# Kernel tuning notes

Measured on AMD Instinct MI355X. Metric: run time of the kernel, lower is better.

The kernel has to match this reference:

```python
import jax, jax.numpy as jnp
import numpy as np

D_MODEL = 512
NUM_HEADS = 8
D_K = D_MODEL // NUM_HEADS
D_FF = 4 * D_MODEL
EPS = 1e-5


def _pos_encoding(seq_len, d_model, dtype=jnp.float32):
    pos = jnp.arange(seq_len, dtype=jnp.float32)[:, None]              # [S,1]
    div = jnp.exp(jnp.arange(0, d_model, 2, dtype=jnp.float32) * (-np.log(10000.0) / d_model))  # [D/2]
    ang = pos * div                                                      # [S,D/2]
    pe = jnp.stack([jnp.sin(ang), jnp.cos(ang)], axis=-1).reshape(seq_len, d_model)
    return pe.astype(dtype)


def _layernorm(x, g, b):
    mu = jnp.mean(x, axis=-1, keepdims=True)
    var = jnp.mean(jnp.square(x - mu), axis=-1, keepdims=True)
    return (x - mu) * jax.lax.rsqrt(var + EPS) * g + b


def setup_inputs() -> dict:
    key = jax.random.key(0)
    ks = jax.random.split(key, 12)
    B, S, D = 4, 2048, D_MODEL
    s = 1.0 / np.sqrt(D)
    inp = {
        "x": jax.random.normal(ks[0], (B, S, D), jnp.float32),
        "Wq": jax.random.normal(ks[1], (D, D), jnp.float32) * s,
        "bq": jnp.zeros((D,), jnp.float32),
        "Wk": jax.random.normal(ks[2], (D, D), jnp.float32) * s,
        "bk": jnp.zeros((D,), jnp.float32),
        "Wv": jax.random.normal(ks[3], (D, D), jnp.float32) * s,
        "bv": jnp.zeros((D,), jnp.float32),
        "Wo": jax.random.normal(ks[4], (D, D), jnp.float32) * s,
        "bo": jnp.zeros((D,), jnp.float32),
        "g1": jnp.ones((D,), jnp.float32),
        "b1": jnp.zeros((D,), jnp.float32),
        "W_ff1": jax.random.normal(ks[5], (D, D_FF), jnp.float32) * s,
        "b_ff1": jnp.zeros((D_FF,), jnp.float32),
        "W_ff2": jax.random.normal(ks[6], (D_FF, D), jnp.float32) * (1.0 / np.sqrt(D_FF)),
        "b_ff2": jnp.zeros((D,), jnp.float32),
        "g2": jnp.ones((D,), jnp.float32),
        "b2": jnp.zeros((D,), jnp.float32),
    }
    return inp


def reference(x, Wq, bq, Wk, bk, Wv, bv, Wo, bo, g1, b1, W_ff1, b_ff1, W_ff2, b_ff2, g2, b2):
    B, S, D = x.shape
    H, dk = NUM_HEADS, D_K
    # positional encoding (deterministic buffer)
    x = x + _pos_encoding(S, D, x.dtype)[None]
    # projections -> [B,H,S,dk]
    q = (x @ Wq + bq).reshape(B, S, H, dk).transpose(0, 2, 1, 3)
    k = (x @ Wk + bk).reshape(B, S, H, dk).transpose(0, 2, 1, 3)
    v = (x @ Wv + bv).reshape(B, S, H, dk).transpose(0, 2, 1, 3)
    # naive attention: materialized [B,H,S,S] scores (as in original)
    scores = jnp.einsum('bhqd,bhkd->bhqk', q, k) / np.sqrt(dk)
    attn = jax.nn.softmax(scores, axis=-1)
    ctx = jnp.einsum('bhqk,bhkd->bhqd', attn, v)
    ctx = ctx.transpose(0, 2, 1, 3).reshape(B, S, D)
    attn_out = ctx @ Wo + bo
    # residual + LN + FFN + residual + LN
    h = _layernorm(x + attn_out, g1, b1)
    ff = jax.nn.relu(h @ W_ff1 + b_ff1) @ W_ff2 + b_ff2
    return _layernorm(h + ff, g2, b2)
```

## Files before the change

kernel.cpp:

```cpp
#include <hip/hip_runtime.h>

typedef unsigned short u16;
typedef unsigned int u32;
typedef __attribute__((ext_vector_type(8))) short s16x8;
typedef __attribute__((ext_vector_type(2))) float f32x2;
typedef __attribute__((ext_vector_type(4))) float f32x4;
typedef __attribute__((ext_vector_type(16))) float f32x16;
typedef __attribute__((ext_vector_type(2))) u32 u32x2;
typedef __attribute__((ext_vector_type(4))) u32 u32x4;

#define MB (1ull << 20)
#define K1SCALE 0.18033688f

__device__ __forceinline__ u16 f2bf(float f) {
  u32 u = __float_as_uint(f);
  u32 r = (u + 0x7fffu + ((u >> 16) & 1u)) >> 16;
  return (u16)r;
}

__device__ __forceinline__ float bf2f(u16 x) { return __uint_as_float(((u32)x) << 16); }

__device__ __forceinline__ u32 cvtpk(float lo, float hi) {
  u32 r;
  asm("v_cvt_pk_bf16_f32 %0, %1, %2" : "=v"(r) : "v"(lo), "v"(hi));
  return r;
}

__device__ __forceinline__ f32x2 pk_add(f32x2 a, f32x2 b) {
  f32x2 d;
  asm("v_pk_add_f32 %0, %1, %2" : "=v"(d) : "v"(a), "v"(b));
  return d;
}

__device__ __forceinline__ void gload16(const u16* g, u16* l) {
  __builtin_amdgcn_global_load_lds((const __attribute__((address_space(1))) void*)g,
                                   (__attribute__((address_space(3))) void*)l, 16, 0, 0);
}

__global__ __launch_bounds__(256) void k_posenc(const float* __restrict__ x,
                                                float* __restrict__ xf, u16* __restrict__ xb) {
  int idx = blockIdx.x * 256 + threadIdx.x;
  int i2 = idx & 255;
  int srow = (idx >> 8) & 2047;
  float div = __expf((float)i2 * -0.03597789207803196f);
  float ang = (float)srow * div;
  f32x2 xv = *(const f32x2*)&x[(size_t)idx * 2];
  float v0 = xv[0] + __sinf(ang);
  float v1 = xv[1] + __cosf(ang);
  *(f32x2*)&xf[(size_t)idx * 2] = (f32x2){v0, v1};
  *(u32*)&xb[(size_t)idx * 2] = cvtpk(v0, v1);
}

__global__ __launch_bounds__(256) void k_wprep(const float* __restrict__ Wq, const float* __restrict__ Wk,
                                               const float* __restrict__ Wv, const float* __restrict__ Wo,
                                               const float* __restrict__ Wff1, const float* __restrict__ Wff2,
                                               const float* __restrict__ bq, const float* __restrict__ bk,
                                               const float* __restrict__ bv,
                                               u16* __restrict__ WqkvT, u16* __restrict__ WoT,
                                               u16* __restrict__ Wff1T, u16* __restrict__ Wff2T,
                                               float* __restrict__ bqkv) {
  __shared__ float tile[32][33];
  int id = blockIdx.x;
  if (id >= 3072) {
    int j = (id - 3072) * 256 + threadIdx.x;
    float v = (j < 512) ? bq[j] * K1SCALE : ((j < 1024) ? bk[j - 512] : bv[j - 1024]);
    bqkv[j] = v;
    return;
  }
  const float* W;
  u16* Wt;
  int K, N, k0, n0;
  float sc = 1.0f;
  if (id < 1024) {
    int mi = id >> 8, t = id & 255;
    K = 512; N = 512;
    k0 = (t & 15) * 32;
    n0 = (t >> 4) * 32;
    if (mi == 0) { W = Wq; Wt = WqkvT; sc = K1SCALE; }
    else if (mi == 1) { W = Wk; Wt = WqkvT + 512 * 512; }
    else if (mi == 2) { W = Wv; Wt = WqkvT + 2 * 512 * 512; }
    else { W = Wo; Wt = WoT; }
  } else if (id < 2048) {
    int t = id - 1024;
    K = 512; N = 2048;
    k0 = (t & 15) * 32;
    n0 = (t >> 4) * 32;
    W = Wff1; Wt = Wff1T;
  } else {
    int t = id - 2048;
    K = 2048; N = 512;
    k0 = (t >> 4) * 32;
    n0 = (t & 15) * 32;
    W = Wff2; Wt = Wff2T;
  }
  int tx = threadIdx.x & 31, ty = threadIdx.x >> 5;
  #pragma unroll
  for (int i = 0; i < 32; i += 8)
    tile[ty + i][tx] = W[(size_t)(k0 + ty + i) * N + n0 + tx];
  __syncthreads();
  #pragma unroll
  for (int i = 0; i < 32; i += 8)
    Wt[(size_t)(n0 + ty + i) * K + k0 + tx] = f2bf(tile[tx][ty + i] * sc);
}

template <int NK, bool RELU, bool QKV, bool F32OUT>
__global__ __launch_bounds__(512, 2) void k_gemm3(const u16* __restrict__ A, const u16* __restrict__ Bt,
                                                  const float* __restrict__ bias, u16* __restrict__ Cb,
                                                  u16* __restrict__ vTout,
                                                  float* __restrict__ Cf0, float* __restrict__ Cf1,
                                                  int N, int lda) {
  constexpr int K = NK * 64;
  __shared__ u16 lA[3][256 * 64];
  __shared__ u16 lB[3][128 * 64];
  int t = threadIdx.x;
  int lane = t & 63;
  int w = t >> 6;
  int wr = w >> 1, wc = w & 1;
  int g = lane >> 4, c = lane & 15;
  size_t tm = (size_t)blockIdx.x * 256;
  size_t tn = (size_t)blockIdx.y * 128;
  A += (size_t)blockIdx.z * K;
  Bt += (size_t)blockIdx.z * K;

  auto stg = [&](int buf, int kt, int half) {
    int k0 = kt * 64;
    #pragma unroll
    for (int i = 0; i < 2; i++) {
      int ch = t + (half * 2 + i) * 512;
      int row = ch >> 3;
      int koff = ((ch ^ row) & 7) << 3;
      gload16(A + (tm + row) * lda + k0 + koff, &lA[buf][ch * 8]);
    }
    int ch = t + half * 512;
    int row = ch >> 3;
    int koff = ((ch ^ row) & 7) << 3;
    gload16(Bt + (tn + row) * lda + k0 + koff, &lB[buf][ch * 8]);
  };

  f32x4 acc[4][4];
  #pragma unroll
  for (int i = 0; i < 4; i++)
    #pragma unroll
    for (int j = 0; j < 4; j++) acc[i][j] = (f32x4){0.f, 0.f, 0.f, 0.f};

  stg(0, 0, 0); stg(0, 0, 1);
  stg(1, 1, 0); stg(1, 1, 1);
  asm volatile("s_waitcnt vmcnt(6)" ::: "memory");
  __builtin_amdgcn_s_barrier();
  __builtin_amdgcn_sched_barrier(0);

  #pragma unroll
  for (int kt = 0; kt < NK; kt++) {
    const int buf = kt % 3;
    const int nb = (kt + 2) % 3;
    s16x8 bfr[4][2], afr[2][2];
    #pragma unroll
    for (int nr = 0; nr < 4; nr++)
      #pragma unroll
      for (int ks = 0; ks < 2; ks++)
        bfr[nr][ks] = *(const s16x8*)&lB[buf][(wc * 64 + nr * 16 + c) * 64 + (((g + 4 * ks) ^ (c & 7)) << 3)];
    #pragma unroll
    for (int mr = 0; mr < 2; mr++)
      #pragma unroll
      for (int ks = 0; ks < 2; ks++)
        afr[mr][ks] = *(const s16x8*)&lA[buf][(wr * 64 + mr * 16 + c) * 64 + (((g + 4 * ks) ^ (c & 7)) << 3)];
    if (kt + 2 < NK) stg(nb, kt + 2, 0);
    __builtin_amdgcn_s_barrier();
    __builtin_amdgcn_sched_barrier(0);
    __builtin_amdgcn_s_setprio(1);
    #pragma unroll
    for (int mr = 0; mr < 2; mr++)
      #pragma unroll
      for (int nr = 0; nr < 4; nr++)
        #pragma unroll
        for (int ks = 0; ks < 2; ks++)
          acc[mr][nr] = __builtin_amdgcn_mfma_f32_16x16x32_bf16(afr[mr][ks], bfr[nr][ks], acc[mr][nr], 0, 0, 0);
    __builtin_amdgcn_s_setprio(0);
    __builtin_amdgcn_s_barrier();
    __builtin_amdgcn_sched_barrier(0);
    #pragma unroll
    for (int mr = 0; mr < 2; mr++)
      #pragma unroll
      for (int ks = 0; ks < 2; ks++)
        afr[mr][ks] = *(const s16x8*)&lA[buf][(wr * 64 + (mr + 2) * 16 + c) * 64 + (((g + 4 * ks) ^ (c & 7)) << 3)];
    if (kt + 2 < NK) stg(nb, kt + 2, 1);
    __builtin_amdgcn_s_barrier();
    __builtin_amdgcn_sched_barrier(0);
    __builtin_amdgcn_s_setprio(1);
    #pragma unroll
    for (int mr = 0; mr < 2; mr++)
      #pragma unroll
      for (int nr = 0; nr < 4; nr++)
        #pragma unroll
        for (int ks = 0; ks < 2; ks++)
          acc[mr + 2][nr] = __builtin_amdgcn_mfma_f32_16x16x32_bf16(afr[mr][ks], bfr[nr][ks], acc[mr + 2][nr], 0, 0, 0);
    __builtin_amdgcn_s_setprio(0);
    if (kt < NK - 1) {
      if (kt + 2 < NK)
        asm volatile("s_waitcnt vmcnt(6)" ::: "memory");
      else
        asm volatile("s_waitcnt vmcnt(0)" ::: "memory");
      __builtin_amdgcn_s_barrier();
      __builtin_amdgcn_sched_barrier(0);
    }
  }

  if (QKV && tn >= 1024) {
    #pragma unroll
    for (int mr = 0; mr < 4; mr++) {
      int row0 = (int)tm + wr * 64 + mr * 16 + g * 4;
      int b = row0 >> 11, s0 = row0 & 2047;
      #pragma unroll
      for (int nr = 0; nr < 4; nr++) {
        int colr = (int)(tn - 1024) + wc * 64 + nr * 16 + c;
        int h = colr >> 6, d = colr & 63;
        float bv = bias[1024 + colr];
        u32 w0 = cvtpk(acc[mr][nr][0] + bv, acc[mr][nr][1] + bv);
        u32 w1 = cvtpk(acc[mr][nr][2] + bv, acc[mr][nr][3] + bv);
        u32x2 pp = {w0, w1};
        *(u32x2*)&vTout[((size_t)((b << 3) + h) * 64 + d) * 2048 + s0] = pp;
      }
    }
  } else if (F32OUT) {
    float* Cf = blockIdx.z ? Cf1 : Cf0;
    bool addb = (blockIdx.z == 0);
    #pragma unroll
    for (int nr = 0; nr < 4; nr++) {
      size_t col = tn + wc * 64 + nr * 16 + c;
      float bv = addb ? bias[col] : 0.0f;
      #pragma unroll
      for (int mr = 0; mr < 4; mr++) {
        size_t row0 = tm + wr * 64 + mr * 16 + g * 4;
        #pragma unroll
        for (int r = 0; r < 4; r++) Cf[(row0 + r) * N + col] = acc[mr][nr][r] + bv;
      }
    }
  } else {
    #pragma unroll
    for (int nr = 0; nr < 4; nr++) {
      size_t col = tn + wc * 64 + nr * 16 + c;
      float bv = bias[col];
      #pragma unroll
      for (int mr = 0; mr < 4; mr++) {
        size_t row0 = tm + wr * 64 + mr * 16 + g * 4;
        #pragma unroll
        for (int r = 0; r < 4; r++) {
          float v = acc[mr][nr][r] + bv;
          if (RELU) v = fmaxf(v, 0.0f);
          Cb[(row0 + r) * N + col] = f2bf(v);
        }
      }
    }
  }
}

template <int BN, bool RELU, bool WF32, bool WBF16>
__global__ __launch_bounds__(256) void k_gemm(const u16* __restrict__ A, const u16* __restrict__ Bt,
                                              const float* __restrict__ bias,
                                              float* __restrict__ Cf, u16* __restrict__ Cb,
                                              int N, int K) {
  constexpr int NACC = BN / 32;
  __shared__ u16 lA[128 * 64];
  __shared__ u16 lB[BN * 64];
  int t = threadIdx.x;
  int lane = t & 63;
  int w = t >> 6;
  int wm = w >> 1, wn = w & 1;
  int g = lane >> 4, c = lane & 15;
  size_t tm = (size_t)blockIdx.x * 128;
  size_t tn = (size_t)blockIdx.y * BN;

  f32x4 acc[4][NACC];
  #pragma unroll
  for (int i = 0; i < 4; i++)
    #pragma unroll
    for (int j = 0; j < NACC; j++) acc[i][j] = (f32x4){0.f, 0.f, 0.f, 0.f};

  for (int k0 = 0; k0 < K; k0 += 64) {
    __syncthreads();
    #pragma unroll
    for (int i = 0; i < 4; i++) {
      int ch = t + i * 256;
      int row = ch >> 3;
      int koff = ((ch ^ row) & 7) << 3;
      gload16(A + (tm + row) * K + k0 + koff, lA + ch * 8);
    }
    #pragma unroll
    for (int i = 0; i < BN / 32; i++) {
      int ch = t + i * 256;
      int row = ch >> 3;
      int koff = ((ch ^ row) & 7) << 3;
      gload16(Bt + (tn + row) * K + k0 + koff, lB + ch * 8);
    }
    __syncthreads();
    #pragma unroll
    for (int kh = 0; kh < 2; kh++) {
      int sl = ((g + 4 * kh) ^ (c & 7)) << 3;
      s16x8 af[4], bf[NACC];
      #pragma unroll
      for (int i = 0; i < 4; i++)
        af[i] = *(const s16x8*)&lA[(wm * 64 + i * 16 + c) * 64 + sl];
      #pragma unroll
      for (int j = 0; j < NACC; j++)
        bf[j] = *(const s16x8*)&lB[(wn * (BN / 2) + j * 16 + c) * 64 + sl];
      #pragma unroll
      for (int i = 0; i < 4; i++)
        #pragma unroll
        for (int j = 0; j < NACC; j++)
          acc[i][j] = __builtin_amdgcn_mfma_f32_16x16x32_bf16(af[i], bf[j], acc[i][j], 0, 0, 0);
    }
  }
  #pragma unroll
  for (int j = 0; j < NACC; j++) {
    size_t col = tn + wn * (BN / 2) + j * 16 + c;
    float bv = bias[col];
    #pragma unroll
    for (int i = 0; i < 4; i++) {
      size_t row0 = tm + wm * 64 + i * 16 + g * 4;
      #pragma unroll
      for (int r = 0; r < 4; r++) {
        float v = acc[i][j][r] + bv;
        if (RELU) v = fmaxf(v, 0.0f);
        if (WF32) Cf[(row0 + r) * N + col] = v;
        if (WBF16) Cb[(row0 + r) * N + col] = f2bf(v);
      }
    }
  }
}

union F16U {
  f32x16 v;
  f32x2 p[8];
};

__global__ __launch_bounds__(512, 4) void k_attn(const u16* __restrict__ qkv,
                                                 const u16* __restrict__ vT,
                                                 u16* __restrict__ ctx) {
  __shared__ u16 lds[8][4096];
  int t = threadIdx.x;
  int w = t >> 6, lane = t & 63;
  int qg = w >> 1, kh = w & 1;
  int ql = lane & 31, hi = lane >> 5;
  int bh = blockIdx.y;
  int b = bh >> 3, h = bh & 7;
  int q0 = blockIdx.x * 128 + qg * 32;
  int r7 = ql & 7;

  int sh = t >> 8;
  int th = t & 255;
  const u16* kbaseg = qkv + (size_t)(b * 2048 + sh * 1024) * 1536 + 512 + h * 64;
  const u16* vbaseg = vT + (size_t)(bh * 64) * 2048 + sh * 1024;

  auto stage = [&](int buf, int step) {
    int t0 = step * 64;
    #pragma unroll
    for (int i = 0; i < 2; i++) {
      int ch = th + i * 256;
      int row = ch >> 3;
      int off = ((ch ^ row) & 7) << 3;
      gload16(kbaseg + (size_t)(t0 + row) * 1536 + off, &lds[(sh * 2 + buf) * 2][ch * 8]);
      gload16(vbaseg + (size_t)row * 2048 + t0 + off, &lds[(sh * 2 + buf) * 2 + 1][ch * 8]);
    }
  };

  const u16* qbase = qkv + (size_t)(b * 2048 + q0 + ql) * 1536 + h * 64 + hi * 8;
  s16x8 qf[4];
  #pragma unroll
  for (int ks = 0; ks < 4; ks++) qf[ks] = *(const s16x8*)(qbase + ks * 16);

  float l = 0.f;
  F16U O0, O1;
  #pragma unroll
  for (int i = 0; i < 16; i++) { O0.v[i] = 0.f; O1.v[i] = 0.f; }

  stage(0, 0);

  for (int step = 0; step < 16; ++step) {
    int buf = step & 1;
    asm volatile("s_waitcnt vmcnt(0)" ::: "memory");
    __builtin_amdgcn_s_barrier();
    __builtin_amdgcn_sched_barrier(0);
    if (step < 15) stage(buf ^ 1, step + 1);

    const u16* lK = lds[(kh * 2 + buf) * 2];
    const u16* lV = lds[(kh * 2 + buf) * 2 + 1];

    F16U S0, S1;
    #pragma unroll
    for (int i = 0; i < 16; i++) { S0.v[i] = 0.f; S1.v[i] = 0.f; }
    #pragma unroll
    for (int ks = 0; ks < 4; ks++) {
      int so = ((ks * 2 + hi) ^ r7) << 3;
      s16x8 kf0 = *(const s16x8*)&lK[ql * 64 + so];
      s16x8 kf1 = *(const s16x8*)&lK[(32 + ql) * 64 + so];
      S0.v = __builtin_amdgcn_mfma_f32_32x32x16_bf16(kf0, qf[ks], S0.v, 0, 0, 0);
      S1.v = __builtin_amdgcn_mfma_f32_32x32x16_bf16(kf1, qf[ks], S1.v, 0, 0, 0);
    }

    #pragma unroll
    for (int i = 0; i < 16; i++) {
      S0.v[i] = __builtin_amdgcn_exp2f(S0.v[i]);
      S1.v[i] = __builtin_amdgcn_exp2f(S1.v[i]);
    }
    f32x2 c0 = pk_add(S0.p[0], S0.p[1]);
    f32x2 c1 = pk_add(S0.p[2], S0.p[3]);
    f32x2 c2 = pk_add(S0.p[4], S0.p[5]);
    f32x2 c3 = pk_add(S0.p[6], S0.p[7]);
    f32x2 d0 = pk_add(S1.p[0], S1.p[1]);
    f32x2 d1 = pk_add(S1.p[2], S1.p[3]);
    f32x2 d2 = pk_add(S1.p[4], S1.p[5]);
    f32x2 d3 = pk_add(S1.p[6], S1.p[7]);
    c0 = pk_add(c0, c1);
    c2 = pk_add(c2, c3);
    d0 = pk_add(d0, d1);
    d2 = pk_add(d2, d3);
    c0 = pk_add(c0, c2);
    d0 = pk_add(d0, d2);
    c0 = pk_add(c0, d0);
    float pssum = c0[0] + c0[1];
    pssum += __shfl_xor(pssum, 32, 64);
    l += pssum;

    auto pv = [&](const f32x16& sv, int kb) {
      u32 a0w = cvtpk(sv[0], sv[1]), a1w = cvtpk(sv[2], sv[3]);
      u32 a2w = cvtpk(sv[4], sv[5]), a3w = cvtpk(sv[6], sv[7]);
      u32 b0w = cvtpk(sv[8], sv[9]), b1w = cvtpk(sv[10], sv[11]);
      u32 b2w = cvtpk(sv[12], sv[13]), b3w = cvtpk(sv[14], sv[15]);
      asm("v_permlane32_swap_b32 %0, %1" : "+v"(a0w), "+v"(a2w));
      asm("v_permlane32_swap_b32 %0, %1" : "+v"(a1w), "+v"(a3w));
      asm("v_permlane32_swap_b32 %0, %1" : "+v"(b0w), "+v"(b2w));
      asm("v_permlane32_swap_b32 %0, %1" : "+v"(b1w), "+v"(b3w));
      u32x4 w0v = {a0w, a1w, a2w, a3w};
      u32x4 w1v = {b0w, b1w, b2w, b3w};
      s16x8 pf0 = __builtin_bit_cast(s16x8, w0v);
      s16x8 pf1 = __builtin_bit_cast(s16x8, w1v);
      int base0 = ((kb * 4 + hi) ^ r7) << 3;
      int base1 = ((kb * 4 + 2 + hi) ^ r7) << 3;
      s16x8 vf00 = *(const s16x8*)&lV[ql * 64 + base0];
      s16x8 vf01 = *(const s16x8*)&lV[ql * 64 + base1];
      s16x8 vf10 = *(const s16x8*)&lV[(32 + ql) * 64 + base0];
      s16x8 vf11 = *(const s16x8*)&lV[(32 + ql) * 64 + base1];
      O0.v = __builtin_amdgcn_mfma_f32_32x32x16_bf16(vf00, pf0, O0.v, 0, 0, 0);
      O0.v = __builtin_amdgcn_mfma_f32_32x32x16_bf16(vf01, pf1, O0.v, 0, 0, 0);
      O1.v = __builtin_amdgcn_mfma_f32_32x32x16_bf16(vf10, pf0, O1.v, 0, 0, 0);
      O1.v = __builtin_amdgcn_mfma_f32_32x32x16_bf16(vf11, pf1, O1.v, 0, 0, 0);
    };
    pv(S0.v, 0);
    pv(S1.v, 1);
  }

  asm volatile("s_waitcnt lgkmcnt(0)" ::: "memory");
  __builtin_amdgcn_s_barrier();
  float* mrg = (float*)&lds[0][0];
  float* p = mrg + (size_t)(qg * 64 + lane) * 34;
  if (kh == 1) {
    p[0] = l;
    #pragma unroll
    for (int i = 0; i < 16; i++) {
      p[1 + i] = O0.v[i];
      p[17 + i] = O1.v[i];
    }
  }
  asm volatile("s_waitcnt lgkmcnt(0)" ::: "memory");
  __builtin_amdgcn_s_barrier();
  if (kh == 0) {
    float inv = 1.0f / (l + p[0]);
    size_t obase = (size_t)(b * 2048 + q0 + ql) * 512 + h * 64;
    #pragma unroll
    for (int k = 0; k < 4; k++) {
      float v0 = (O0.v[4 * k] + p[1 + 4 * k]) * inv;
      float v1 = (O0.v[4 * k + 1] + p[1 + 4 * k + 1]) * inv;
      float v2 = (O0.v[4 * k + 2] + p[1 + 4 * k + 2]) * inv;
      float v3 = (O0.v[4 * k + 3] + p[1 + 4 * k + 3]) * inv;
      u32x2 p0 = {cvtpk(v0, v1), cvtpk(v2, v3)};
      *(u32x2*)&ctx[obase + 8 * k + 4 * hi] = p0;
      float u0 = (O1.v[4 * k] + p[17 + 4 * k]) * inv;
      float u1 = (O1.v[4 * k + 1] + p[17 + 4 * k + 1]) * inv;
      float u2 = (O1.v[4 * k + 2] + p[17 + 4 * k + 2]) * inv;
      float u3 = (O1.v[4 * k + 3] + p[17 + 4 * k + 3]) * inv;
      u32x2 p1 = {cvtpk(u0, u1), cvtpk(u2, u3)};
      *(u32x2*)&ctx[obase + 32 + 8 * k + 4 * hi] = p1;
    }
  }
}

template <bool WB>
__global__ __launch_bounds__(256) void k_addln(const float* __restrict__ A, const float* __restrict__ Bv,
                                               const float* __restrict__ G, const float* __restrict__ Bb,
                                               float* __restrict__ Of, u16* __restrict__ Ob) {
  int row = blockIdx.x;
  int t = threadIdx.x;
  size_t base = (size_t)row * 512 + 2 * t;
  f32x2 av = *(const f32x2*)&A[base];
  f32x2 bv = *(const f32x2*)&Bv[base];
  float x0 = av[0] + bv[0];
  float x1 = av[1] + bv[1];
  float s = x0 + x1;
  #pragma unroll
  for (int d = 1; d < 64; d <<= 1) s += __shfl_xor(s, d, 64);
  __shared__ float red[8];
  int w = t >> 6, lane = t & 63;
  if (lane == 0) red[w] = s;
  __syncthreads();
  float mu = (red[0] + red[1] + red[2] + red[3]) * (1.0f / 512.0f);
  float d0 = x0 - mu, d1 = x1 - mu;
  float vs = d0 * d0 + d1 * d1;
  #pragma unroll
  for (int d = 1; d < 64; d <<= 1) vs += __shfl_xor(vs, d, 64);
  if (lane == 0) red[4 + w] = vs;
  __syncthreads();
  float var = (red[4] + red[5] + red[6] + red[7]) * (1.0f / 512.0f);
  float rs = rsqrtf(var + 1e-5f);
  f32x2 gg = *(const f32x2*)&G[2 * t];
  f32x2 bb = *(const f32x2*)&Bb[2 * t];
  float o0 = d0 * rs * gg[0] + bb[0];
  float o1 = d1 * rs * gg[1] + bb[1];
  *(f32x2*)&Of[base] = (f32x2){o0, o1};
  if (WB) *(u32*)&Ob[base] = cvtpk(o0, o1);
}

__global__ __launch_bounds__(256) void k_addln3(const float* __restrict__ A, const float* __restrict__ B1,
                                                const float* __restrict__ B2,
                                                const float* __restrict__ G, const float* __restrict__ Bb,
                                                float* __restrict__ Of) {
  int row = blockIdx.x;
  int t = threadIdx.x;
  size_t base = (size_t)row * 512 + 2 * t;
  f32x2 av = *(const f32x2*)&A[base];
  f32x2 b1v = *(const f32x2*)&B1[base];
  f32x2 b2v = *(const f32x2*)&B2[base];
  float x0 = av[0] + b1v[0] + b2v[0];
  float x1 = av[1] + b1v[1] + b2v[1];
  float s = x0 + x1;
  #pragma unroll
  for (int d = 1; d < 64; d <<= 1) s += __shfl_xor(s, d, 64);
  __shared__ float red[8];
  int w = t >> 6, lane = t & 63;
  if (lane == 0) red[w] = s;
  __syncthreads();
  float mu = (red[0] + red[1] + red[2] + red[3]) * (1.0f / 512.0f);
  float d0 = x0 - mu, d1 = x1 - mu;
  float vs = d0 * d0 + d1 * d1;
  #pragma unroll
  for (int d = 1; d < 64; d <<= 1) vs += __shfl_xor(vs, d, 64);
  if (lane == 0) red[4 + w] = vs;
  __syncthreads();
  float var = (red[4] + red[5] + red[6] + red[7]) * (1.0f / 512.0f);
  float rs = rsqrtf(var + 1e-5f);
  f32x2 gg = *(const f32x2*)&G[2 * t];
  f32x2 bb = *(const f32x2*)&Bb[2 * t];
  float o0 = d0 * rs * gg[0] + bb[0];
  float o1 = d1 * rs * gg[1] + bb[1];
  *(f32x2*)&Of[base] = (f32x2){o0, o1};
}

extern "C" void kernel_launch(void* const* d_in, const int* in_sizes, int n_in,
                              void* d_out, int out_size, void* d_ws, size_t ws_size,
                              hipStream_t stream) {
  const float* x = (const float*)d_in[0];
  const float* Wq = (const float*)d_in[1];
  const float* bq = (const float*)d_in[2];
  const float* Wk = (const float*)d_in[3];
  const float* bk = (const float*)d_in[4];
  const float* Wv = (const float*)d_in[5];
  const float* bv = (const float*)d_in[6];
  const float* Wo = (const float*)d_in[7];
  const float* bo = (const float*)d_in[8];
  const float* g1 = (const float*)d_in[9];
  const float* b1 = (const float*)d_in[10];
  const float* Wff1 = (const float*)d_in[11];
  const float* bff1 = (const float*)d_in[12];
  const float* Wff2 = (const float*)d_in[13];
  const float* bff2 = (const float*)d_in[14];
  const float* g2 = (const float*)d_in[15];
  const float* b2 = (const float*)d_in[16];

  char* ws = (char*)d_ws;
  float* xpe_f = (float*)(ws + 0);
  float* ao2 = (float*)(ws + 0);
  u16* xpe_b = (u16*)(ws + 16 * MB);
  u16* qkv = (u16*)(ws + 24 * MB);
  u16* vT = (u16*)(ws + 48 * MB);
  u16* ctx = (u16*)(ws + 56 * MB);
  float* ao = (float*)(ws + 64 * MB);
  float* hf = (float*)(ws + 80 * MB);
  u16* hb = (u16*)(ws + 96 * MB);
  u16* ff1 = (u16*)(ws + 24 * MB);
  u16* WqkvT = (u16*)(ws + 104 * MB);
  u16* WoT = (u16*)(ws + 106 * MB);
  u16* Wff1T = (u16*)(ws + 107 * MB);
  u16* Wff2T = (u16*)(ws + 109 * MB);
  float* bqkv = (float*)(ws + 111 * MB);
  (void)in_sizes; (void)n_in; (void)out_size; (void)ws_size;

  k_posenc<<<8192, 256, 0, stream>>>(x, xpe_f, xpe_b);
  k_wprep<<<3078, 256, 0, stream>>>(Wq, Wk, Wv, Wo, Wff1, Wff2, bq, bk, bv,
                                    WqkvT, WoT, Wff1T, Wff2T, bqkv);

  k_gemm3<8, false, true, false><<<dim3(32, 12), 512, 0, stream>>>(xpe_b, WqkvT, bqkv, qkv, vT,
                                                                   nullptr, nullptr, 1536, 512);
  k_attn<<<dim3(16, 32), 512, 0, stream>>>(qkv, vT, ctx);
  k_gemm<64, false, true, false><<<dim3(64, 8), 256, 0, stream>>>(ctx, WoT, bo, ao, nullptr, 512, 512);
  k_addln<true><<<8192, 256, 0, stream>>>(xpe_f, ao, g1, b1, hf, hb);
  k_gemm3<8, true, false, false><<<dim3(32, 16), 512, 0, stream>>>(hb, Wff1T, bff1, ff1, nullptr,
                                                                   nullptr, nullptr, 2048, 512);
  k_gemm3<16, false, false, true><<<dim3(32, 4, 2), 512, 0, stream>>>(ff1, Wff2T, bff2, nullptr, nullptr,
                                                                      ao, ao2, 512, 2048);
  k_addln3<<<8192, 256, 0, stream>>>(hf, ao, ao2, g2, b2, (float*)d_out);
}
```

Baseline: 175.9 us.

## Merge prep kernels and remap workgroup IDs for XCD-aware L2 locality

Merges the positional-encoding and weight-prep kernels into a single launch, removing one kernel launch. Remaps the flat workgroup index in the GEMM and attention kernels so that consecutive logical tiles land on the same XCD, since blocks are dispatched round-robin across the eight XCDs on MI300-class parts. Blocks that share A/B rows or K/V heads should then hit the same L2. The remap assumes the grid size is divisible by 8, and the attention remap hardcodes 512 blocks.

```diff
diff --git a/kernel.cpp b/kernel.cpp
--- a/kernel.cpp
+++ b/kernel.cpp
@@ -18,8 +18,6 @@
   return (u16)r;
 }
 
-__device__ __forceinline__ float bf2f(u16 x) { return __uint_as_float(((u32)x) << 16); }
-
 __device__ __forceinline__ u32 cvtpk(float lo, float hi) {
   u32 r;
   asm("v_cvt_pk_bf16_f32 %0, %1, %2" : "=v"(r) : "v"(lo), "v"(hi));
@@ -37,30 +35,32 @@
                                    (__attribute__((address_space(3))) void*)l, 16, 0, 0);
 }
 
-__global__ __launch_bounds__(256) void k_posenc(const float* __restrict__ x,
-                                                float* __restrict__ xf, u16* __restrict__ xb) {
-  int idx = blockIdx.x * 256 + threadIdx.x;
-  int i2 = idx & 255;
-  int srow = (idx >> 8) & 2047;
-  float div = __expf((float)i2 * -0.03597789207803196f);
-  float ang = (float)srow * div;
-  f32x2 xv = *(const f32x2*)&x[(size_t)idx * 2];
-  float v0 = xv[0] + __sinf(ang);
-  float v1 = xv[1] + __cosf(ang);
-  *(f32x2*)&xf[(size_t)idx * 2] = (f32x2){v0, v1};
-  *(u32*)&xb[(size_t)idx * 2] = cvtpk(v0, v1);
-}
-
-__global__ __launch_bounds__(256) void k_wprep(const float* __restrict__ Wq, const float* __restrict__ Wk,
-                                               const float* __restrict__ Wv, const float* __restrict__ Wo,
-                                               const float* __restrict__ Wff1, const float* __restrict__ Wff2,
-                                               const float* __restrict__ bq, const float* __restrict__ bk,
-                                               const float* __restrict__ bv,
-                                               u16* __restrict__ WqkvT, u16* __restrict__ WoT,
-                                               u16* __restrict__ Wff1T, u16* __restrict__ Wff2T,
-                                               float* __restrict__ bqkv) {
+__global__ __launch_bounds__(256) void k_prep(const float* __restrict__ x,
+                                              float* __restrict__ xf, u16* __restrict__ xb,
+                                              const float* __restrict__ Wq, const float* __restrict__ Wk,
+                                              const float* __restrict__ Wv, const float* __restrict__ Wo,
+                                              const float* __restrict__ Wff1, const float* __restrict__ Wff2,
+                                              const float* __restrict__ bq, const float* __restrict__ bk,
+                                              const float* __restrict__ bv,
+                                              u16* __restrict__ WqkvT, u16* __restrict__ WoT,
+                                              u16* __restrict__ Wff1T, u16* __restrict__ Wff2T,
+                                              float* __restrict__ bqkv) {
   __shared__ float tile[32][33];
-  int id = blockIdx.x;
+  int bid = blockIdx.x;
+  if (bid < 8192) {
+    int idx = bid * 256 + threadIdx.x;
+    int i2 = idx & 255;
+    int srow = (idx >> 8) & 2047;
+    float div = __expf((float)i2 * -0.03597789207803196f);
+    float ang = (float)srow * div;
+    f32x2 xv = *(const f32x2*)&x[(size_t)idx * 2];
+    float v0 = xv[0] + __sinf(ang);
+    float v1 = xv[1] + __cosf(ang);
+    *(f32x2*)&xf[(size_t)idx * 2] = (f32x2){v0, v1};
+    *(u32*)&xb[(size_t)idx * 2] = cvtpk(v0, v1);
+    return;
+  }
+  int id = bid - 8192;
   if (id >= 3072) {
     int j = (id - 3072) * 256 + threadIdx.x;
     float v = (j < 512) ? bq[j] * K1SCALE : ((j < 1024) ? bk[j - 512] : bv[j - 1024]);
@@ -117,8 +117,13 @@
   int w = t >> 6;
   int wr = w >> 1, wc = w & 1;
   int g = lane >> 4, c = lane & 15;
-  size_t tm = (size_t)blockIdx.x * 256;
-  size_t tn = (size_t)blockIdx.y * 128;
+  int nwg = gridDim.x * gridDim.y;
+  int fid = blockIdx.y * gridDim.x + blockIdx.x;
+  int wid = (fid & 7) * (nwg >> 3) + (fid >> 3);
+  int bx = wid / gridDim.y;
+  int by = wid % gridDim.y;
+  size_t tm = (size_t)bx * 256;
+  size_t tn = (size_t)by * 128;
   A += (size_t)blockIdx.z * K;
   Bt += (size_t)blockIdx.z * K;
 
@@ -267,8 +272,13 @@
   int w = t >> 6;
   int wm = w >> 1, wn = w & 1;
   int g = lane >> 4, c = lane & 15;
-  size_t tm = (size_t)blockIdx.x * 128;
-  size_t tn = (size_t)blockIdx.y * BN;
+  int nwg = gridDim.x * gridDim.y;
+  int fid = blockIdx.y * gridDim.x + blockIdx.x;
+  int wid = (fid & 7) * (nwg >> 3) + (fid >> 3);
+  int bx = wid / gridDim.y;
+  int by = wid % gridDim.y;
+  size_t tm = (size_t)bx * 128;
+  size_t tn = (size_t)by * BN;
 
   f32x4 acc[4][NACC];
   #pragma unroll
@@ -341,9 +351,12 @@
   int w = t >> 6, lane = t & 63;
   int qg = w >> 1, kh = w & 1;
   int ql = lane & 31, hi = lane >> 5;
-  int bh = blockIdx.y;
+  int bid = blockIdx.x;
+  int wid = (bid & 7) * 64 + (bid >> 3);
+  int bx = wid & 15;
+  int bh = wid >> 4;
   int b = bh >> 3, h = bh & 7;
-  int q0 = blockIdx.x * 128 + qg * 32;
+  int q0 = bx * 128 + qg * 32;
   int r7 = ql & 7;
 
   int sh = t >> 8;
@@ -593,13 +606,12 @@
   float* bqkv = (float*)(ws + 111 * MB);
   (void)in_sizes; (void)n_in; (void)out_size; (void)ws_size;
 
-  k_posenc<<<8192, 256, 0, stream>>>(x, xpe_f, xpe_b);
-  k_wprep<<<3078, 256, 0, stream>>>(Wq, Wk, Wv, Wo, Wff1, Wff2, bq, bk, bv,
-                                    WqkvT, WoT, Wff1T, Wff2T, bqkv);
+  k_prep<<<11270, 256, 0, stream>>>(x, xpe_f, xpe_b, Wq, Wk, Wv, Wo, Wff1, Wff2,
+                                    bq, bk, bv, WqkvT, WoT, Wff1T, Wff2T, bqkv);
 
   k_gemm3<8, false, true, false><<<dim3(32, 12), 512, 0, stream>>>(xpe_b, WqkvT, bqkv, qkv, vT,
                                                                    nullptr, nullptr, 1536, 512);
-  k_attn<<<dim3(16, 32), 512, 0, stream>>>(qkv, vT, ctx);
+  k_attn<<<512, 512, 0, stream>>>(qkv, vT, ctx);
   k_gemm<64, false, true, false><<<dim3(64, 8), 256, 0, stream>>>(ctx, WoT, bo, ao, nullptr, 512, 512);
   k_addln<true><<<8192, 256, 0, stream>>>(xpe_f, ao, g1, b1, hf, hb);
   k_gemm3<8, true, false, false><<<dim3(32, 16), 512, 0, stream>>>(hb, Wff1T, bff1, ff1, nullptr,
```

Result: faster. 171.5 us (median of 3 runs) (-2.5%).
